# Kernel tuning notes

Measured on AMD Instinct MI355X. Metric: run time of the kernel, lower is better.

Reference implementation:

```python
import jax, jax.numpy as jnp
import numpy as np

NUM_EXPERTS = 3
SCALING = 8.0 / 8.0  # alpha / r


def setup_inputs() -> dict:
    key = jax.random.key(0)
    ks = jax.random.split(key, 8)
    B, H, W, D = 64, 28, 28, 512
    Dh = 4 * D
    E, K, R = 3, 2, 8
    T = B * H * W
    x = jax.random.normal(ks[0], (B, H, W, D), dtype=jnp.float32)
    W1 = jax.random.normal(ks[1], (D, Dh), dtype=jnp.float32) * (1.0 / D ** 0.5)
    b1 = jnp.zeros((Dh,), dtype=jnp.float32)
    W2 = jax.random.normal(ks[2], (Dh, D), dtype=jnp.float32) * (1.0 / Dh ** 0.5)
    b2 = jnp.zeros((D,), dtype=jnp.float32)
    w_down = jax.random.normal(ks[3], (E, D, R), dtype=jnp.float32) * (1.0 / D ** 0.5)
    # original init is zeros; use small randn so output/grads are non-trivial
    w_up = jax.random.normal(ks[4], (E, R, D), dtype=jnp.float32) * 0.02
    gate_logits = jax.random.normal(ks[5], (T, E), dtype=jnp.float32)
    gate_probs = jax.nn.softmax(gate_logits, axis=-1)
    topk_probs, topk_indices = jax.lax.top_k(gate_probs, K)
    topk_indices = topk_indices.astype(jnp.int64)
    return {"x": x, "W1": W1, "b1": b1, "W2": W2, "b2": b2,
            "w_down": w_down, "w_up": w_up, "gate_probs": gate_probs,
            "topk_probs": topk_probs, "topk_indices": topk_indices}


def reference(x, W1, b1, W2, b2, w_down, w_up, gate_probs, topk_probs, topk_indices):
    # frozen base ConvNeXt MLP (channels-last): Linear -> GELU -> Linear
    orig_out = jax.nn.gelu(jnp.dot(x, W1) + b1, approximate=False) @ W2 + b2

    D = x.shape[-1]
    x_flat = x.reshape(-1, D)  # [T, D]

    # dense per-expert LoRA over all tokens (rank-8, cheap), then mask-combine
    down = jnp.einsum('td,edr->etr', x_flat, w_down)          # [E, T, r]
    up = jnp.einsum('etr,erd->etd', jax.nn.gelu(down, approximate=False), w_up) * SCALING  # [E, T, D]

    # weights[e, t] = sum_k topk_probs[t, k] * (topk_indices[t, k] == e)
    E = w_down.shape[0]
    mask = (topk_indices[None, :, :] == jnp.arange(E)[:, None, None])  # [E, T, K]
    weights = jnp.sum(jnp.where(mask, topk_probs[None], 0.0), axis=-1)  # [E, T]

    moe_out = jnp.einsum('et,etd->td', weights, up).reshape(x.shape)
    return orig_out + moe_out
```

## Files before the change

### kernel.cpp

```cpp
#include <hip/hip_runtime.h>

typedef _Float16 f16;
typedef _Float16 f16x8 __attribute__((ext_vector_type(8)));
typedef _Float16 f16x4 __attribute__((ext_vector_type(4)));
typedef float f32x4 __attribute__((ext_vector_type(4)));

#define TD 512
#define TDH 2048

__device__ __forceinline__ float gelu_fast(float x) {
  float u = x * fmaf(x * x, 0.0713548162f, 1.595769122f);
  float e = __expf(-u);
  return x * __builtin_amdgcn_rcpf(1.0f + e);
}

__device__ __forceinline__ void glds16(const f16* g, f16* l) {
  __builtin_amdgcn_global_load_lds(
      (const __attribute__((address_space(1))) void*)g,
      (__attribute__((address_space(3))) void*)l, 16, 0, 0);
}

__global__ __launch_bounds__(256) void k_conv_x(f16* __restrict__ dst,
                                                const float* __restrict__ src,
                                                int n4) {
  int i = blockIdx.x * 256 + threadIdx.x;
  if (i >= n4) return;
  float4 v = ((const float4*)src)[i];
  f16x4 o = {(f16)v.x, (f16)v.y, (f16)v.z, (f16)v.w};
  ((f16x4*)dst)[i] = o;
}

__global__ void k_trans(f16* __restrict__ dst, const float* __restrict__ src,
                        int R, int C) {
  __shared__ float t[32][33];
  const int bx = blockIdx.x, by = blockIdx.y;
  const int tx = threadIdx.x, ty = threadIdx.y;
#pragma unroll
  for (int s = 0; s < 32; s += 8)
    t[ty + s][tx] = src[(size_t)(by * 32 + ty + s) * C + bx * 32 + tx];
  __syncthreads();
#pragma unroll
  for (int s = 0; s < 32; s += 8)
    dst[(size_t)(bx * 32 + ty + s) * R + by * 32 + tx] = (f16)t[tx][ty + s];
}

__global__ __launch_bounds__(256) void k_wdT(f16* __restrict__ dst,
                                             const float* __restrict__ wd) {
  int i = blockIdx.x * 256 + threadIdx.x;
  int n = i >> 9, k = i & 511;
  float v = (n < 24) ? wd[(size_t)((n >> 3) * 512 + k) * 8 + (n & 7)] : 0.0f;
  dst[i] = (f16)v;
}

__global__ __launch_bounds__(256) void k_wuT(f16* __restrict__ dst,
                                             const float* __restrict__ wu) {
  int i = blockIdx.x * 256 + threadIdx.x;
  int d = i >> 5, er = i & 31;
  float v = (er < 24) ? wu[(size_t)(er >> 3) * 4096 + (er & 7) * 512 + d] : 0.0f;
  dst[i] = (f16)v;
}

template <int EPI>
__global__ __launch_bounds__(256) void k_gemm(
    const f16* __restrict__ A, const f16* __restrict__ B, int Kt, int lda,
    int ldb, const float* __restrict__ bias, f16* __restrict__ Hout, int ldh,
    float* __restrict__ Out, int ldc, const float* __restrict__ tkp,
    const int* __restrict__ tki, const f16* __restrict__ Ag,
    const f16* __restrict__ Bg) {
  __shared__ __align__(16) f16 As[2][128 * 32];
  __shared__ __align__(16) f16 Bs[2][128 * 32];
  const int tid = threadIdx.x;
  const int lane = tid & 63;
  const int w = tid >> 6;
  const int wm = w >> 1, wn = w & 1;
  const int bm = blockIdx.x, bn = blockIdx.y;

  const int c0 = 2 * w;
  const int lrow = lane >> 2;
  const int srow = c0 * 16 + lrow;
  const int skk = ((lane & 3) ^ ((lrow >> 1) & 3)) * 8;
  const f16* gA = A + (size_t)(bm * 128 + srow) * lda + skk;
  const f16* gB = B + (size_t)(bn * 128 + srow) * ldb + skk;
  f16* lA0 = &As[0][c0 * 512];
  f16* lA1 = &As[1][c0 * 512];
  f16* lB0 = &Bs[0][c0 * 512];
  f16* lB1 = &Bs[1][c0 * 512];

  f32x4 acc[4][4] = {};

  const int frow = lane & 15;
  const int swk = (((lane >> 4) ^ ((frow >> 1) & 3))) * 8;

  const int nt = Kt / 32;

  glds16(gA, lA0);
  glds16(gA + (size_t)16 * lda, lA0 + 512);
  glds16(gB, lB0);
  glds16(gB + (size_t)16 * ldb, lB0 + 512);
  __syncthreads();

  for (int t = 0; t < nt; ++t) {
    f16* dA = (t & 1) ? lA0 : lA1;
    f16* dB = (t & 1) ? lB0 : lB1;
    if (t + 1 < nt) {
      const int k = (t + 1) * 32;
      glds16(gA + k, dA);
      glds16(gA + k + (size_t)16 * lda, dA + 512);
      glds16(gB + k, dB);
      glds16(gB + k + (size_t)16 * ldb, dB + 512);
    } else if (EPI == 1) {
      const f16* gAg = Ag + (size_t)(bm * 128 + srow) * 32 + skk;
      const f16* gBg = Bg + (size_t)(bn * 128 + srow) * 32 + skk;
      glds16(gAg, dA);
      glds16(gAg + 512, dA + 512);
      glds16(gBg, dB);
      glds16(gBg + 512, dB + 512);
    }
    const f16* rA = As[t & 1];
    const f16* rB = Bs[t & 1];
    f16x8 af[4], bf[4];
#pragma unroll
    for (int i = 0; i < 4; i++)
      af[i] = *(const f16x8*)&rA[(wm * 64 + i * 16 + frow) * 32 + swk];
#pragma unroll
    for (int j = 0; j < 4; j++)
      bf[j] = *(const f16x8*)&rB[(wn * 64 + j * 16 + frow) * 32 + swk];
#pragma unroll
    for (int i = 0; i < 4; i++)
#pragma unroll
      for (int j = 0; j < 4; j++)
        acc[i][j] = __builtin_amdgcn_mfma_f32_16x16x32_f16(bf[j], af[i],
                                                           acc[i][j], 0, 0, 0);
    __syncthreads();
  }

  if constexpr (EPI == 1) {
    const f16* rA = As[nt & 1];
    const f16* rB = Bs[nt & 1];
    f16x8 af[4], bf[4];
#pragma unroll
    for (int i = 0; i < 4; i++)
      af[i] = *(const f16x8*)&rA[(wm * 64 + i * 16 + frow) * 32 + swk];
#pragma unroll
    for (int j = 0; j < 4; j++)
      bf[j] = *(const f16x8*)&rB[(wn * 64 + j * 16 + frow) * 32 + swk];
#pragma unroll
    for (int i = 0; i < 4; i++)
#pragma unroll
      for (int j = 0; j < 4; j++)
        acc[i][j] = __builtin_amdgcn_mfma_f32_16x16x32_f16(bf[j], af[i],
                                                           acc[i][j], 0, 0, 0);
  }

  const int m0 = wm * 64 + (lane & 15);
  const int n0 = wn * 64 + ((lane >> 4) << 2);

  if constexpr (EPI == 0) {
#pragma unroll
    for (int i = 0; i < 4; i++) {
      const size_t rb = (size_t)(bm * 128 + m0 + i * 16) * ldh + bn * 128 + n0;
#pragma unroll
      for (int j = 0; j < 4; j++) {
        const float4 bb = *(const float4*)&bias[bn * 128 + n0 + j * 16];
        f16x4 o = {(f16)gelu_fast(acc[i][j][0] + bb.x),
                   (f16)gelu_fast(acc[i][j][1] + bb.y),
                   (f16)gelu_fast(acc[i][j][2] + bb.z),
                   (f16)gelu_fast(acc[i][j][3] + bb.w)};
        *(f16x4*)&Hout[rb + j * 16] = o;
      }
    }
  } else if constexpr (EPI == 1) {
#pragma unroll
    for (int i = 0; i < 4; i++) {
      const size_t rb = (size_t)(bm * 128 + m0 + i * 16) * ldc + bn * 128 + n0;
#pragma unroll
      for (int j = 0; j < 4; j++) {
        const float4 bb = *(const float4*)&bias[bn * 128 + n0 + j * 16];
        float4 v = {acc[i][j][0] + bb.x, acc[i][j][1] + bb.y,
                    acc[i][j][2] + bb.z, acc[i][j][3] + bb.w};
        *(float4*)&Out[rb + j * 16] = v;
      }
    }
  } else {
    if (wn == 0) {
#pragma unroll
      for (int i = 0; i < 4; i++) {
        const int m = bm * 128 + m0 + i * 16;
        const int i0 = tki[m * 2], i1 = tki[m * 2 + 1];
        const float p0 = tkp[m * 2], p1 = tkp[m * 2 + 1];
#pragma unroll
        for (int j = 0; j < 2; j++) {
          const int nb = n0 + j * 16;
          const int e = nb >> 3;
          const float wgt = (i0 == e ? p0 : 0.0f) + (i1 == e ? p1 : 0.0f);
          f16x4 o = {(f16)(wgt * gelu_fast(acc[i][j][0])),
                     (f16)(wgt * gelu_fast(acc[i][j][1])),
                     (f16)(wgt * gelu_fast(acc[i][j][2])),
                     (f16)(wgt * gelu_fast(acc[i][j][3]))};
          *(f16x4*)&Hout[(size_t)m * 32 + nb] = o;
        }
      }
    }
  }
}

extern "C" void kernel_launch(void* const* d_in, const int* in_sizes, int n_in,
                              void* d_out, int out_size, void* d_ws,
                              size_t ws_size, hipStream_t stream) {
  const float* x = (const float*)d_in[0];
  const float* W1 = (const float*)d_in[1];
  const float* b1 = (const float*)d_in[2];
  const float* W2 = (const float*)d_in[3];
  const float* b2 = (const float*)d_in[4];
  const float* wd = (const float*)d_in[5];
  const float* wu = (const float*)d_in[6];
  const float* tkp = (const float*)d_in[8];
  const int* tki = (const int*)d_in[9];
  float* out = (float*)d_out;

  const int T = in_sizes[0] / TD;

  char* p = (char*)d_ws;
  f16* W1T = (f16*)p; p += (size_t)TDH * TD * sizeof(f16);
  f16* W2T = (f16*)p; p += (size_t)TD * TDH * sizeof(f16);
  f16* wdT = (f16*)p; p += (size_t)128 * TD * sizeof(f16);
  f16* wuT = (f16*)p; p += (size_t)TD * 32 * sizeof(f16);
  size_t fixed = (size_t)(p - (char*)d_ws);
  const size_t per_tok = (size_t)(TD + TDH + 32) * sizeof(f16);
  long mc = (long)((ws_size > fixed ? ws_size - fixed : 0) / per_tok);
  if (mc > T) mc = T;
  mc = (mc / 128) * 128;
  if (mc < 128) mc = 128;
  f16* xb = (f16*)p; p += (size_t)mc * TD * sizeof(f16);
  f16* Hb = (f16*)p; p += (size_t)mc * TDH * sizeof(f16);
  f16* gb = (f16*)p;

  k_trans<<<dim3(TDH / 32, TD / 32), dim3(32, 8), 0, stream>>>(W1T, W1, TD, TDH);
  k_trans<<<dim3(TD / 32, TDH / 32), dim3(32, 8), 0, stream>>>(W2T, W2, TDH, TD);
  k_wdT<<<dim3(65536 / 256), 256, 0, stream>>>(wdT, wd);
  k_wuT<<<dim3(16384 / 256), 256, 0, stream>>>(wuT, wu);

  for (long off = 0; off < T; off += mc) {
    long m = T - off;
    if (m > mc) m = mc;
    const int mt = (int)(m / 128);
    const int n4 = (int)(m * TD / 4);
    k_conv_x<<<dim3((n4 + 255) / 256), 256, 0, stream>>>(xb, x + off * TD, n4);
    k_gemm<2><<<dim3(mt, 1), 256, 0, stream>>>(xb, wdT, TD, TD, TD, nullptr,
                                               gb, 32, nullptr, 0,
                                               tkp + off * 2, tki + off * 2,
                                               nullptr, nullptr);
    k_gemm<0><<<dim3(mt, TDH / 128), 256, 0, stream>>>(
        xb, W1T, TD, TD, TD, b1, Hb, TDH, nullptr, 0, nullptr, nullptr,
        nullptr, nullptr);
    k_gemm<1><<<dim3(mt, TD / 128), 256, 0, stream>>>(
        Hb, W2T, TDH, TDH, TDH, b2, nullptr, 0, out + off * TD, TD, nullptr,
        nullptr, gb, wuT);
  }
}
```

Baseline: 564.8 us.

## Use 256x256 tiled 512-thread GEMM with triple-buffered LDS for the MLP GEMMs

Adds a new GEMM kernel with 256x256 output tiles, 8 waves per block and a three-stage global_load_lds pipeline synchronised by explicit vmcnt waits and barriers. It replaces the 128x128 double-buffered kernel for the W1 (GELU) and W2 (+LoRA up) GEMMs, and swaps the grid order so N tiles vary fastest. The aim is more data reuse per LDS load and better latency hiding. The cost is higher register pressure (128 accumulator floats per thread), 96 KB of LDS, and fewer blocks per chunk. The old kernel is kept only for the rank-32 LoRA down projection.

```diff
diff --git a/kernel.cpp b/kernel.cpp
--- a/kernel.cpp
+++ b/kernel.cpp
@@ -19,6 +19,11 @@
       (const __attribute__((address_space(1))) void*)g,
       (__attribute__((address_space(3))) void*)l, 16, 0, 0);
 }
+
+#define WAITB(N) \
+  asm volatile("s_waitcnt vmcnt(" #N ")\n\ts_barrier" ::: "memory")
+#define DRAINB() \
+  asm volatile("s_waitcnt lgkmcnt(0)\n\ts_barrier" ::: "memory")
 
 __global__ __launch_bounds__(256) void k_conv_x(f16* __restrict__ dst,
                                                 const float* __restrict__ src,
@@ -61,12 +66,129 @@
 }
 
 template <int EPI>
+__global__ __launch_bounds__(512) void k_gemm256(
+    const f16* __restrict__ A, const f16* __restrict__ B, int nt, int lda,
+    int ldb, const float* __restrict__ bias, f16* __restrict__ Hout, int ldh,
+    float* __restrict__ Out, int ldc, const f16* __restrict__ Ag,
+    const f16* __restrict__ Bg) {
+  __shared__ __align__(16) f16 As[3][8192];
+  __shared__ __align__(16) f16 Bs[3][8192];
+  const int tid = threadIdx.x;
+  const int lane = tid & 63;
+  const int w = tid >> 6;
+  const int wm = w >> 2;
+  const int wn = w & 3;
+  const int bn = blockIdx.x, bm = blockIdx.y;
+
+  const int lrow = tid >> 2;
+  const int scol = ((tid & 3) ^ ((lrow >> 1) & 3)) * 8;
+  const f16* pA0 = A + (size_t)(bm * 256 + lrow) * lda + scol;
+  const f16* pA1 = pA0 + (size_t)128 * lda;
+  const f16* pB0 = B + (size_t)(bn * 256 + lrow) * ldb + scol;
+  const f16* pB1 = pB0 + (size_t)128 * ldb;
+  const f16* qA0 = nullptr; const f16* qA1 = nullptr;
+  const f16* qB0 = nullptr; const f16* qB1 = nullptr;
+  if constexpr (EPI == 1) {
+    qA0 = Ag + (size_t)(bm * 256 + lrow) * 32 + scol;
+    qA1 = qA0 + 128 * 32;
+    qB0 = Bg + (size_t)(bn * 256 + lrow) * 32 + scol;
+    qB1 = qB0 + 128 * 32;
+  }
+  const int dbase = w * 512;
+
+  const int ntt = nt + (EPI == 1 ? 1 : 0);
+
+#define STAGE(S, BUF)                                                   \
+  do {                                                                  \
+    f16* dA = &As[BUF][dbase];                                          \
+    f16* dB = &Bs[BUF][dbase];                                          \
+    if ((S) < nt) {                                                     \
+      const size_t o = (size_t)(S) * 32;                                \
+      glds16(pA0 + o, dA); glds16(pA1 + o, dA + 4096);                  \
+      glds16(pB0 + o, dB); glds16(pB1 + o, dB + 4096);                  \
+    } else {                                                            \
+      glds16(qA0, dA); glds16(qA1, dA + 4096);                          \
+      glds16(qB0, dB); glds16(qB1, dB + 4096);                          \
+    }                                                                   \
+  } while (0)
+
+  f32x4 acc[8][4] = {};
+  const int frow = lane & 15;
+  const int swk = (((lane >> 4) ^ ((frow >> 1) & 3))) * 8;
+
+#define COMPUTE(BUF)                                                        \
+  do {                                                                      \
+    const f16* rA = &As[BUF][(wm * 128 + frow) * 32 + swk];                 \
+    const f16* rB = &Bs[BUF][(wn * 64 + frow) * 32 + swk];                  \
+    f16x8 af[8], bf[4];                                                     \
+    _Pragma("unroll") for (int i = 0; i < 8; i++)                           \
+        af[i] = *(const f16x8*)&rA[i * 512];                                \
+    _Pragma("unroll") for (int j = 0; j < 4; j++)                           \
+        bf[j] = *(const f16x8*)&rB[j * 512];                                \
+    _Pragma("unroll") for (int i = 0; i < 8; i++)                           \
+        _Pragma("unroll") for (int j = 0; j < 4; j++)                       \
+            acc[i][j] = __builtin_amdgcn_mfma_f32_16x16x32_f16(             \
+                bf[j], af[i], acc[i][j], 0, 0, 0);                          \
+  } while (0)
+
+  STAGE(0, 0);
+  STAGE(1, 1);
+  STAGE(2, 2);
+
+  int buf = 0;
+  for (int t = 0; t < ntt - 2; ++t) {
+    WAITB(8);
+    COMPUTE(buf);
+    DRAINB();
+    if (t + 3 < ntt) STAGE(t + 3, buf);
+    buf = (buf == 2) ? 0 : buf + 1;
+  }
+  WAITB(4);
+  COMPUTE(buf);
+  DRAINB();
+  buf = (buf == 2) ? 0 : buf + 1;
+  WAITB(0);
+  COMPUTE(buf);
+
+  const int m0 = wm * 128 + (lane & 15);
+  const int n0 = wn * 64 + ((lane >> 4) << 2);
+
+  if constexpr (EPI == 0) {
+#pragma unroll
+    for (int i = 0; i < 8; i++) {
+      const size_t rb = (size_t)(bm * 256 + m0 + i * 16) * ldh + bn * 256 + n0;
+#pragma unroll
+      for (int j = 0; j < 4; j++) {
+        const float4 bb = *(const float4*)&bias[bn * 256 + n0 + j * 16];
+        f16x4 o = {(f16)gelu_fast(acc[i][j][0] + bb.x),
+                   (f16)gelu_fast(acc[i][j][1] + bb.y),
+                   (f16)gelu_fast(acc[i][j][2] + bb.z),
+                   (f16)gelu_fast(acc[i][j][3] + bb.w)};
+        *(f16x4*)&Hout[rb + j * 16] = o;
+      }
+    }
+  } else {
+#pragma unroll
+    for (int i = 0; i < 8; i++) {
+      const size_t rb = (size_t)(bm * 256 + m0 + i * 16) * ldc + bn * 256 + n0;
+#pragma unroll
+      for (int j = 0; j < 4; j++) {
+        const float4 bb = *(const float4*)&bias[bn * 256 + n0 + j * 16];
+        float4 v = {acc[i][j][0] + bb.x, acc[i][j][1] + bb.y,
+                    acc[i][j][2] + bb.z, acc[i][j][3] + bb.w};
+        *(float4*)&Out[rb + j * 16] = v;
+      }
+    }
+  }
+#undef STAGE
+#undef COMPUTE
+}
+
+template <int EPI>
 __global__ __launch_bounds__(256) void k_gemm(
     const f16* __restrict__ A, const f16* __restrict__ B, int Kt, int lda,
-    int ldb, const float* __restrict__ bias, f16* __restrict__ Hout, int ldh,
-    float* __restrict__ Out, int ldc, const float* __restrict__ tkp,
-    const int* __restrict__ tki, const f16* __restrict__ Ag,
-    const f16* __restrict__ Bg) {
+    int ldb, f16* __restrict__ Hout, const float* __restrict__ tkp,
+    const int* __restrict__ tki) {
   __shared__ __align__(16) f16 As[2][128 * 32];
   __shared__ __align__(16) f16 Bs[2][128 * 32];
   const int tid = threadIdx.x;
@@ -87,10 +209,8 @@
   f16* lB1 = &Bs[1][c0 * 512];
 
   f32x4 acc[4][4] = {};
-
   const int frow = lane & 15;
   const int swk = (((lane >> 4) ^ ((frow >> 1) & 3))) * 8;
-
   const int nt = Kt / 32;
 
   glds16(gA, lA0);
@@ -108,13 +228,6 @@
       glds16(gA + k + (size_t)16 * lda, dA + 512);
       glds16(gB + k, dB);
       glds16(gB + k + (size_t)16 * ldb, dB + 512);
-    } else if (EPI == 1) {
-      const f16* gAg = Ag + (size_t)(bm * 128 + srow) * 32 + skk;
-      const f16* gBg = Bg + (size_t)(bn * 128 + srow) * 32 + skk;
-      glds16(gAg, dA);
-      glds16(gAg + 512, dA + 512);
-      glds16(gBg, dB);
-      glds16(gBg + 512, dB + 512);
     }
     const f16* rA = As[t & 1];
     const f16* rB = Bs[t & 1];
@@ -134,71 +247,24 @@
     __syncthreads();
   }
 
-  if constexpr (EPI == 1) {
-    const f16* rA = As[nt & 1];
-    const f16* rB = Bs[nt & 1];
-    f16x8 af[4], bf[4];
-#pragma unroll
-    for (int i = 0; i < 4; i++)
-      af[i] = *(const f16x8*)&rA[(wm * 64 + i * 16 + frow) * 32 + swk];
-#pragma unroll
-    for (int j = 0; j < 4; j++)
-      bf[j] = *(const f16x8*)&rB[(wn * 64 + j * 16 + frow) * 32 + swk];
-#pragma unroll
-    for (int i = 0; i < 4; i++)
-#pragma unroll
-      for (int j = 0; j < 4; j++)
-        acc[i][j] = __builtin_amdgcn_mfma_f32_16x16x32_f16(bf[j], af[i],
-                                                           acc[i][j], 0, 0, 0);
-  }
-
   const int m0 = wm * 64 + (lane & 15);
   const int n0 = wn * 64 + ((lane >> 4) << 2);
-
-  if constexpr (EPI == 0) {
+  if (wn == 0) {
 #pragma unroll
     for (int i = 0; i < 4; i++) {
-      const size_t rb = (size_t)(bm * 128 + m0 + i * 16) * ldh + bn * 128 + n0;
-#pragma unroll
-      for (int j = 0; j < 4; j++) {
-        const float4 bb = *(const float4*)&bias[bn * 128 + n0 + j * 16];
-        f16x4 o = {(f16)gelu_fast(acc[i][j][0] + bb.x),
-                   (f16)gelu_fast(acc[i][j][1] + bb.y),
-                   (f16)gelu_fast(acc[i][j][2] + bb.z),
-                   (f16)gelu_fast(acc[i][j][3] + bb.w)};
-        *(f16x4*)&Hout[rb + j * 16] = o;
-      }
-    }
-  } else if constexpr (EPI == 1) {
-#pragma unroll
-    for (int i = 0; i < 4; i++) {
-      const size_t rb = (size_t)(bm * 128 + m0 + i * 16) * ldc + bn * 128 + n0;
-#pragma unroll
-      for (int j = 0; j < 4; j++) {
-        const float4 bb = *(const float4*)&bias[bn * 128 + n0 + j * 16];
-        float4 v = {acc[i][j][0] + bb.x, acc[i][j][1] + bb.y,
-                    acc[i][j][2] + bb.z, acc[i][j][3] + bb.w};
-        *(float4*)&Out[rb + j * 16] = v;
-      }
-    }
-  } else {
-    if (wn == 0) {
-#pragma unroll
-      for (int i = 0; i < 4; i++) {
-        const int m = bm * 128 + m0 + i * 16;
-        const int i0 = tki[m * 2], i1 = tki[m * 2 + 1];
-        const float p0 = tkp[m * 2], p1 = tkp[m * 2 + 1];
-#pragma unroll
-        for (int j = 0; j < 2; j++) {
-          const int nb = n0 + j * 16;
-          const int e = nb >> 3;
-          const float wgt = (i0 == e ? p0 : 0.0f) + (i1 == e ? p1 : 0.0f);
-          f16x4 o = {(f16)(wgt * gelu_fast(acc[i][j][0])),
-                     (f16)(wgt * gelu_fast(acc[i][j][1])),
-                     (f16)(wgt * gelu_fast(acc[i][j][2])),
-                     (f16)(wgt * gelu_fast(acc[i][j][3]))};
-          *(f16x4*)&Hout[(size_t)m * 32 + nb] = o;
-        }
+      const int m = bm * 128 + m0 + i * 16;
+      const int i0 = tki[m * 2], i1 = tki[m * 2 + 1];
+      const float p0 = tkp[m * 2], p1 = tkp[m * 2 + 1];
+#pragma unroll
+      for (int j = 0; j < 2; j++) {
+        const int nb = n0 + j * 16;
+        const int e = nb >> 3;
+        const float wgt = (i0 == e ? p0 : 0.0f) + (i1 == e ? p1 : 0.0f);
+        f16x4 o = {(f16)(wgt * gelu_fast(acc[i][j][0])),
+                   (f16)(wgt * gelu_fast(acc[i][j][1])),
+                   (f16)(wgt * gelu_fast(acc[i][j][2])),
+                   (f16)(wgt * gelu_fast(acc[i][j][3]))};
+        *(f16x4*)&Hout[(size_t)m * 32 + nb] = o;
       }
     }
   }
@@ -229,8 +295,8 @@
   const size_t per_tok = (size_t)(TD + TDH + 32) * sizeof(f16);
   long mc = (long)((ws_size > fixed ? ws_size - fixed : 0) / per_tok);
   if (mc > T) mc = T;
-  mc = (mc / 128) * 128;
-  if (mc < 128) mc = 128;
+  mc = (mc / 256) * 256;
+  if (mc < 256) mc = 256;
   f16* xb = (f16*)p; p += (size_t)mc * TD * sizeof(f16);
   f16* Hb = (f16*)p; p += (size_t)mc * TDH * sizeof(f16);
   f16* gb = (f16*)p;
@@ -243,18 +309,16 @@
   for (long off = 0; off < T; off += mc) {
     long m = T - off;
     if (m > mc) m = mc;
-    const int mt = (int)(m / 128);
+    const int mt1 = (int)(m / 128);
+    const int mt2 = (int)(m / 256);
     const int n4 = (int)(m * TD / 4);
     k_conv_x<<<dim3((n4 + 255) / 256), 256, 0, stream>>>(xb, x + off * TD, n4);
-    k_gemm<2><<<dim3(mt, 1), 256, 0, stream>>>(xb, wdT, TD, TD, TD, nullptr,
-                                               gb, 32, nullptr, 0,
-                                               tkp + off * 2, tki + off * 2,
-                                               nullptr, nullptr);
-    k_gemm<0><<<dim3(mt, TDH / 128), 256, 0, stream>>>(
-        xb, W1T, TD, TD, TD, b1, Hb, TDH, nullptr, 0, nullptr, nullptr,
-        nullptr, nullptr);
-    k_gemm<1><<<dim3(mt, TD / 128), 256, 0, stream>>>(
-        Hb, W2T, TDH, TDH, TDH, b2, nullptr, 0, out + off * TD, TD, nullptr,
-        nullptr, gb, wuT);
-  }
-}
+    k_gemm<2><<<dim3(mt1, 1), 256, 0, stream>>>(xb, wdT, TD, TD, TD, gb,
+                                                tkp + off * 2, tki + off * 2);
+    k_gemm256<0><<<dim3(TDH / 256, mt2), 512, 0, stream>>>(
+        xb, W1T, TD / 32, TD, TD, b1, Hb, TDH, nullptr, 0, nullptr, nullptr);
+    k_gemm256<1><<<dim3(TD / 256, mt2), 512, 0, stream>>>(
+        Hb, W2T, TDH / 32, TDH, TDH, b2, nullptr, 0, out + off * TD, TD, gb,
+        wuT);
+  }
+}
```

After: 622.3 us. 10.2% more time.

## Replace main GEMMs with 256x256 8-wave ping-pong pipelined kernel and XCD swizzle

Applied to the files above, without the earlier changes.

Replaces the 128x128 double-buffered GEMM used for the two large MLP matmuls with a 512-thread, 256x256-tile kernel. It splits each 64-wide K step into half-tiles, interleaves LDS reads, async global-to-LDS loads and MFMA quarter-blocks behind explicit vmcnt waits and barriers, and raises wave priority around the MFMA bursts. Block indices are remapped so neighbouring tiles land on the same XCD. The LoRA up-projection tail is padded to K=64 so it fits the new K step, which means the lora-down kernel now writes zero padding. The changes target latency hiding and reuse per byte loaded, at the cost of hand-tuned wait counts that are fragile, and the token chunk size must now be a multiple of 256.

```diff
diff --git a/kernel.cpp b/kernel.cpp
--- a/kernel.cpp
+++ b/kernel.cpp
@@ -19,6 +19,19 @@
       (const __attribute__((address_space(1))) void*)g,
       (__attribute__((address_space(3))) void*)l, 16, 0, 0);
 }
+
+#define VW6_BAR()                                          \
+  do {                                                     \
+    asm volatile("s_waitcnt vmcnt(6)" ::: "memory");       \
+    __builtin_amdgcn_s_barrier();                          \
+  } while (0)
+#define VW0_BAR()                                          \
+  do {                                                     \
+    asm volatile("s_waitcnt vmcnt(0)" ::: "memory");       \
+    __builtin_amdgcn_s_barrier();                          \
+  } while (0)
+#define BAR() __builtin_amdgcn_s_barrier()
+#define LGKM0() asm volatile("s_waitcnt lgkmcnt(0)" ::: "memory")
 
 __global__ __launch_bounds__(256) void k_conv_x(f16* __restrict__ dst,
                                                 const float* __restrict__ src,
@@ -55,42 +68,198 @@
 __global__ __launch_bounds__(256) void k_wuT(f16* __restrict__ dst,
                                              const float* __restrict__ wu) {
   int i = blockIdx.x * 256 + threadIdx.x;
-  int d = i >> 5, er = i & 31;
+  int d = i >> 6, er = i & 63;
   float v = (er < 24) ? wu[(size_t)(er >> 3) * 4096 + (er & 7) * 512 + d] : 0.0f;
   dst[i] = (f16)v;
 }
 
 template <int EPI>
-__global__ __launch_bounds__(256) void k_gemm(
+__global__ __launch_bounds__(512, 2) void k_gemm8p(
+    const f16* __restrict__ A, const f16* __restrict__ B, int ntm, int NT,
+    int lda, int ldb, const float* __restrict__ bias, f16* __restrict__ Hout,
+    int ldh, float* __restrict__ Out, int ldc, const f16* __restrict__ Ag,
+    const f16* __restrict__ Bg, int nbn) {
+  __shared__ __align__(16) f16 LA[2][2][8192];
+  __shared__ __align__(16) f16 LB[2][2][8192];
+  const int tid = threadIdx.x;
+  const int lane = tid & 63;
+  const int w = tid >> 6;
+  const int wm = w >> 2, wn = w & 3;
+
+  const int nwg = gridDim.x;
+  const int q = nwg >> 3, r = nwg & 7;
+  const int xcd = blockIdx.x & 7, pos = blockIdx.x >> 3;
+  const int swz =
+      (xcd < r ? xcd * (q + 1) : r * (q + 1) + (xcd - r) * q) + pos;
+  const int bm = swz / nbn, bn = swz - bm * nbn;
+
+  const int lrow = tid >> 2;
+  const int scol = ((tid & 3) ^ ((lrow >> 1) & 3)) * 8;
+  const f16* pA = A + (size_t)(bm * 256 + lrow) * lda + scol;
+  const f16* pB = B + (size_t)(bn * 256 + lrow) * ldb + scol;
+  const f16* qA =
+      (EPI == 1) ? Ag + (size_t)(bm * 256 + lrow) * 64 + scol : nullptr;
+  const f16* qB =
+      (EPI == 1) ? Bg + (size_t)(bn * 256 + lrow) * 64 + scol : nullptr;
+  const int dbase = w * 512;
+  const size_t ldas = (size_t)128 * lda, ldbs = (size_t)128 * ldb;
+
+#define STG_A(S, H, BUF)                                             \
+  do {                                                               \
+    if ((S) < NT) {                                                  \
+      f16* d0 = &LA[BUF][H][dbase];                                  \
+      if ((S) < ntm) {                                               \
+        const f16* s_ = pA + (size_t)(S)*64 + (H)*32;                \
+        glds16(s_, d0);                                              \
+        glds16(s_ + ldas, d0 + 4096);                                \
+      } else {                                                       \
+        const f16* s_ = qA + (H)*32;                                 \
+        glds16(s_, d0);                                              \
+        glds16(s_ + 128 * 64, d0 + 4096);                            \
+      }                                                              \
+    }                                                                \
+  } while (0)
+#define STG_B(S, H, BUF)                                             \
+  do {                                                               \
+    if ((S) < NT) {                                                  \
+      f16* d0 = &LB[BUF][H][dbase];                                  \
+      if ((S) < ntm) {                                               \
+        const f16* s_ = pB + (size_t)(S)*64 + (H)*32;                \
+        glds16(s_, d0);                                              \
+        glds16(s_ + ldbs, d0 + 4096);                                \
+      } else {                                                       \
+        const f16* s_ = qB + (H)*32;                                 \
+        glds16(s_, d0);                                              \
+        glds16(s_ + 128 * 64, d0 + 4096);                            \
+      }                                                              \
+    }                                                                \
+  } while (0)
+
+  f32x4 acc[8][4] = {};
+  f16x8 af[8], bf[4];
+  const int frow = lane & 15;
+  const int swk = ((lane >> 4) ^ ((frow >> 1) & 3)) * 8;
+  const int aoff = (wm * 128 + frow) * 32 + swk;
+  const int boff = (wn * 64 + frow) * 32 + swk;
+
+#define DS_AF(BUF, H)                                           \
+  _Pragma("unroll") for (int i = 0; i < 8; i++) af[i] =         \
+      *(const f16x8*)&LA[BUF][H][aoff + i * 512];
+#define DS_BF(BUF, H, J0)                                       \
+  bf[J0] = *(const f16x8*)&LB[BUF][H][boff + (J0)*512];         \
+  bf[(J0) + 1] = *(const f16x8*)&LB[BUF][H][boff + ((J0) + 1) * 512];
+#define MFQ(NQ)                                                         \
+  __builtin_amdgcn_s_setprio(1);                                        \
+  _Pragma("unroll") for (int i = 0; i < 8; i++) {                       \
+    acc[i][2 * (NQ)] = __builtin_amdgcn_mfma_f32_16x16x32_f16(          \
+        bf[2 * (NQ)], af[i], acc[i][2 * (NQ)], 0, 0, 0);                \
+    acc[i][2 * (NQ) + 1] = __builtin_amdgcn_mfma_f32_16x16x32_f16(      \
+        bf[2 * (NQ) + 1], af[i], acc[i][2 * (NQ) + 1], 0, 0, 0);        \
+  }                                                                     \
+  __builtin_amdgcn_s_setprio(0);
+
+#define ITER(I, W4, W8)                                                    \
+  do {                                                                     \
+    const int t0 = 2 * (I), t1 = t0 + 1;                                   \
+     DS_AF(0, 0); DS_BF(0, 0, 0); STG_B(t1, 1, 1);                  \
+    BAR(); LGKM0(); MFQ(0); BAR();                                         \
+     DS_BF(0, 0, 2); STG_A(t0 + 2, 0, 0);                           \
+    BAR(); LGKM0(); MFQ(1); BAR();                                         \
+     DS_AF(0, 1); DS_BF(0, 1, 0); STG_B(t0 + 2, 0, 0);              \
+    BAR(); LGKM0(); MFQ(0); BAR();                                         \
+     DS_BF(0, 1, 2); STG_A(t0 + 2, 1, 0);                           \
+    W4(); LGKM0(); MFQ(1); BAR();                                          \
+     DS_AF(1, 0); DS_BF(1, 0, 0); STG_B(t0 + 2, 1, 0);              \
+    BAR(); LGKM0(); MFQ(0); BAR();                                         \
+     DS_BF(1, 0, 2); STG_A(t1 + 2, 0, 1);                           \
+    BAR(); LGKM0(); MFQ(1); BAR();                                         \
+     DS_AF(1, 1); DS_BF(1, 1, 0); STG_B(t1 + 2, 0, 1);              \
+    BAR(); LGKM0(); MFQ(0); BAR();                                         \
+     DS_BF(1, 1, 2); STG_A(t1 + 2, 1, 1);                           \
+    W8(); LGKM0(); MFQ(1); BAR();                                          \
+  } while (0)
+
+  STG_A(0, 0, 0); STG_B(0, 0, 0); STG_A(0, 1, 0); STG_B(0, 1, 0);
+  STG_A(1, 0, 1); STG_B(1, 0, 1); STG_A(1, 1, 1);
+  VW6_BAR();
+
+  const int NIT = NT >> 1;
+#pragma unroll 1
+  for (int i = 0; i + 1 < NIT; ++i) ITER(i, VW6_BAR, VW6_BAR);
+  if constexpr (EPI == 0) {
+    ITER(NIT - 1, VW0_BAR, VW0_BAR);
+  } else {
+    ITER(NIT - 1, VW6_BAR, VW0_BAR);
+    DS_AF(0, 0); DS_BF(0, 0, 0); LGKM0(); MFQ(0);
+    DS_BF(0, 0, 2); LGKM0(); MFQ(1);
+    DS_AF(0, 1); DS_BF(0, 1, 0); LGKM0(); MFQ(0);
+    DS_BF(0, 1, 2); LGKM0(); MFQ(1);
+  }
+
+  const int m0 = wm * 128 + (lane & 15);
+  const int n0 = wn * 64 + ((lane >> 4) << 2);
+
+  if constexpr (EPI == 0) {
+#pragma unroll
+    for (int i = 0; i < 8; i++) {
+      const size_t rb = (size_t)(bm * 256 + m0 + i * 16) * ldh + bn * 256 + n0;
+#pragma unroll
+      for (int j = 0; j < 4; j++) {
+        const float4 bb = *(const float4*)&bias[bn * 256 + n0 + j * 16];
+        f16x4 o = {(f16)gelu_fast(acc[i][j][0] + bb.x),
+                   (f16)gelu_fast(acc[i][j][1] + bb.y),
+                   (f16)gelu_fast(acc[i][j][2] + bb.z),
+                   (f16)gelu_fast(acc[i][j][3] + bb.w)};
+        *(f16x4*)&Hout[rb + j * 16] = o;
+      }
+    }
+  } else {
+#pragma unroll
+    for (int i = 0; i < 8; i++) {
+      const size_t rb = (size_t)(bm * 256 + m0 + i * 16) * ldc + bn * 256 + n0;
+#pragma unroll
+      for (int j = 0; j < 4; j++) {
+        const float4 bb = *(const float4*)&bias[bn * 256 + n0 + j * 16];
+        float4 v = {acc[i][j][0] + bb.x, acc[i][j][1] + bb.y,
+                    acc[i][j][2] + bb.z, acc[i][j][3] + bb.w};
+        *(float4*)&Out[rb + j * 16] = v;
+      }
+    }
+  }
+#undef STG_A
+#undef STG_B
+#undef DS_AF
+#undef DS_BF
+#undef MFQ
+#undef ITER
+}
+
+__global__ __launch_bounds__(256) void k_lora_down(
     const f16* __restrict__ A, const f16* __restrict__ B, int Kt, int lda,
-    int ldb, const float* __restrict__ bias, f16* __restrict__ Hout, int ldh,
-    float* __restrict__ Out, int ldc, const float* __restrict__ tkp,
-    const int* __restrict__ tki, const f16* __restrict__ Ag,
-    const f16* __restrict__ Bg) {
+    int ldb, f16* __restrict__ Gout, const float* __restrict__ tkp,
+    const int* __restrict__ tki) {
   __shared__ __align__(16) f16 As[2][128 * 32];
   __shared__ __align__(16) f16 Bs[2][128 * 32];
   const int tid = threadIdx.x;
   const int lane = tid & 63;
   const int w = tid >> 6;
   const int wm = w >> 1, wn = w & 1;
-  const int bm = blockIdx.x, bn = blockIdx.y;
+  const int bm = blockIdx.x;
 
   const int c0 = 2 * w;
   const int lrow = lane >> 2;
   const int srow = c0 * 16 + lrow;
   const int skk = ((lane & 3) ^ ((lrow >> 1) & 3)) * 8;
   const f16* gA = A + (size_t)(bm * 128 + srow) * lda + skk;
-  const f16* gB = B + (size_t)(bn * 128 + srow) * ldb + skk;
+  const f16* gB = B + (size_t)srow * ldb + skk;
   f16* lA0 = &As[0][c0 * 512];
   f16* lA1 = &As[1][c0 * 512];
   f16* lB0 = &Bs[0][c0 * 512];
   f16* lB1 = &Bs[1][c0 * 512];
 
   f32x4 acc[4][4] = {};
-
   const int frow = lane & 15;
-  const int swk = (((lane >> 4) ^ ((frow >> 1) & 3))) * 8;
-
+  const int swk = ((lane >> 4) ^ ((frow >> 1) & 3)) * 8;
   const int nt = Kt / 32;
 
   glds16(gA, lA0);
@@ -108,13 +277,6 @@
       glds16(gA + k + (size_t)16 * lda, dA + 512);
       glds16(gB + k, dB);
       glds16(gB + k + (size_t)16 * ldb, dB + 512);
-    } else if (EPI == 1) {
-      const f16* gAg = Ag + (size_t)(bm * 128 + srow) * 32 + skk;
-      const f16* gBg = Bg + (size_t)(bn * 128 + srow) * 32 + skk;
-      glds16(gAg, dA);
-      glds16(gAg + 512, dA + 512);
-      glds16(gBg, dB);
-      glds16(gBg + 512, dB + 512);
     }
     const f16* rA = As[t & 1];
     const f16* rB = Bs[t & 1];
@@ -134,71 +296,26 @@
     __syncthreads();
   }
 
-  if constexpr (EPI == 1) {
-    const f16* rA = As[nt & 1];
-    const f16* rB = Bs[nt & 1];
-    f16x8 af[4], bf[4];
-#pragma unroll
-    for (int i = 0; i < 4; i++)
-      af[i] = *(const f16x8*)&rA[(wm * 64 + i * 16 + frow) * 32 + swk];
-#pragma unroll
-    for (int j = 0; j < 4; j++)
-      bf[j] = *(const f16x8*)&rB[(wn * 64 + j * 16 + frow) * 32 + swk];
-#pragma unroll
-    for (int i = 0; i < 4; i++)
-#pragma unroll
-      for (int j = 0; j < 4; j++)
-        acc[i][j] = __builtin_amdgcn_mfma_f32_16x16x32_f16(bf[j], af[i],
-                                                           acc[i][j], 0, 0, 0);
-  }
-
   const int m0 = wm * 64 + (lane & 15);
   const int n0 = wn * 64 + ((lane >> 4) << 2);
-
-  if constexpr (EPI == 0) {
+  if (wn == 0) {
 #pragma unroll
     for (int i = 0; i < 4; i++) {
-      const size_t rb = (size_t)(bm * 128 + m0 + i * 16) * ldh + bn * 128 + n0;
-#pragma unroll
-      for (int j = 0; j < 4; j++) {
-        const float4 bb = *(const float4*)&bias[bn * 128 + n0 + j * 16];
-        f16x4 o = {(f16)gelu_fast(acc[i][j][0] + bb.x),
-                   (f16)gelu_fast(acc[i][j][1] + bb.y),
-                   (f16)gelu_fast(acc[i][j][2] + bb.z),
-                   (f16)gelu_fast(acc[i][j][3] + bb.w)};
-        *(f16x4*)&Hout[rb + j * 16] = o;
-      }
-    }
-  } else if constexpr (EPI == 1) {
-#pragma unroll
-    for (int i = 0; i < 4; i++) {
-      const size_t rb = (size_t)(bm * 128 + m0 + i * 16) * ldc + bn * 128 + n0;
-#pragma unroll
-      for (int j = 0; j < 4; j++) {
-        const float4 bb = *(const float4*)&bias[bn * 128 + n0 + j * 16];
-        float4 v = {acc[i][j][0] + bb.x, acc[i][j][1] + bb.y,
-                    acc[i][j][2] + bb.z, acc[i][j][3] + bb.w};
-        *(float4*)&Out[rb + j * 16] = v;
-      }
-    }
-  } else {
-    if (wn == 0) {
-#pragma unroll
-      for (int i = 0; i < 4; i++) {
-        const int m = bm * 128 + m0 + i * 16;
-        const int i0 = tki[m * 2], i1 = tki[m * 2 + 1];
-        const float p0 = tkp[m * 2], p1 = tkp[m * 2 + 1];
-#pragma unroll
-        for (int j = 0; j < 2; j++) {
-          const int nb = n0 + j * 16;
-          const int e = nb >> 3;
-          const float wgt = (i0 == e ? p0 : 0.0f) + (i1 == e ? p1 : 0.0f);
-          f16x4 o = {(f16)(wgt * gelu_fast(acc[i][j][0])),
-                     (f16)(wgt * gelu_fast(acc[i][j][1])),
-                     (f16)(wgt * gelu_fast(acc[i][j][2])),
-                     (f16)(wgt * gelu_fast(acc[i][j][3]))};
-          *(f16x4*)&Hout[(size_t)m * 32 + nb] = o;
-        }
+      const int m = bm * 128 + m0 + i * 16;
+      const int i0 = tki[m * 2], i1 = tki[m * 2 + 1];
+      const float p0 = tkp[m * 2], p1 = tkp[m * 2 + 1];
+#pragma unroll
+      for (int j = 0; j < 2; j++) {
+        const int nb = n0 + j * 16;
+        const int e = nb >> 3;
+        const float wgt = (i0 == e ? p0 : 0.0f) + (i1 == e ? p1 : 0.0f);
+        f16x4 o = {(f16)(wgt * gelu_fast(acc[i][j][0])),
+                   (f16)(wgt * gelu_fast(acc[i][j][1])),
+                   (f16)(wgt * gelu_fast(acc[i][j][2])),
+                   (f16)(wgt * gelu_fast(acc[i][j][3]))};
+        *(f16x4*)&Gout[(size_t)m * 64 + nb] = o;
+        f16x4 z = {(f16)0.f, (f16)0.f, (f16)0.f, (f16)0.f};
+        *(f16x4*)&Gout[(size_t)m * 64 + nb + 32] = z;
       }
     }
   }
@@ -224,37 +341,38 @@
   f16* W1T = (f16*)p; p += (size_t)TDH * TD * sizeof(f16);
   f16* W2T = (f16*)p; p += (size_t)TD * TDH * sizeof(f16);
   f16* wdT = (f16*)p; p += (size_t)128 * TD * sizeof(f16);
-  f16* wuT = (f16*)p; p += (size_t)TD * 32 * sizeof(f16);
+  f16* wuT = (f16*)p; p += (size_t)TD * 64 * sizeof(f16);
   size_t fixed = (size_t)(p - (char*)d_ws);
-  const size_t per_tok = (size_t)(TD + TDH + 32) * sizeof(f16);
+  const size_t per_tok = (size_t)(TD + TDH + 64) * sizeof(f16);
   long mc = (long)((ws_size > fixed ? ws_size - fixed : 0) / per_tok);
   if (mc > T) mc = T;
-  mc = (mc / 128) * 128;
-  if (mc < 128) mc = 128;
+  mc = (mc / 256) * 256;
+  if (mc < 256) mc = 256;
   f16* xb = (f16*)p; p += (size_t)mc * TD * sizeof(f16);
   f16* Hb = (f16*)p; p += (size_t)mc * TDH * sizeof(f16);
   f16* gb = (f16*)p;
 
-  k_trans<<<dim3(TDH / 32, TD / 32), dim3(32, 8), 0, stream>>>(W1T, W1, TD, TDH);
-  k_trans<<<dim3(TD / 32, TDH / 32), dim3(32, 8), 0, stream>>>(W2T, W2, TDH, TD);
+  k_trans<<<dim3(TDH / 32, TD / 32), dim3(32, 8), 0, stream>>>(W1T, W1, TD,
+                                                               TDH);
+  k_trans<<<dim3(TD / 32, TDH / 32), dim3(32, 8), 0, stream>>>(W2T, W2, TDH,
+                                                               TD);
   k_wdT<<<dim3(65536 / 256), 256, 0, stream>>>(wdT, wd);
-  k_wuT<<<dim3(16384 / 256), 256, 0, stream>>>(wuT, wu);
+  k_wuT<<<dim3(32768 / 256), 256, 0, stream>>>(wuT, wu);
 
   for (long off = 0; off < T; off += mc) {
     long m = T - off;
     if (m > mc) m = mc;
-    const int mt = (int)(m / 128);
+    const int mt1 = (int)(m / 128);
+    const int mt2 = (int)(m / 256);
     const int n4 = (int)(m * TD / 4);
     k_conv_x<<<dim3((n4 + 255) / 256), 256, 0, stream>>>(xb, x + off * TD, n4);
-    k_gemm<2><<<dim3(mt, 1), 256, 0, stream>>>(xb, wdT, TD, TD, TD, nullptr,
-                                               gb, 32, nullptr, 0,
-                                               tkp + off * 2, tki + off * 2,
-                                               nullptr, nullptr);
-    k_gemm<0><<<dim3(mt, TDH / 128), 256, 0, stream>>>(
-        xb, W1T, TD, TD, TD, b1, Hb, TDH, nullptr, 0, nullptr, nullptr,
-        nullptr, nullptr);
-    k_gemm<1><<<dim3(mt, TD / 128), 256, 0, stream>>>(
-        Hb, W2T, TDH, TDH, TDH, b2, nullptr, 0, out + off * TD, TD, nullptr,
-        nullptr, gb, wuT);
-  }
-}
+    k_lora_down<<<dim3(mt1), 256, 0, stream>>>(xb, wdT, TD, TD, TD, gb,
+                                               tkp + off * 2, tki + off * 2);
+    k_gemm8p<0><<<dim3(mt2 * (TDH / 256)), 512, 0, stream>>>(
+        xb, W1T, TD / 64, TD / 64, TD, TD, b1, Hb, TDH, nullptr, 0, nullptr,
+        nullptr, TDH / 256);
+    k_gemm8p<1><<<dim3(mt2 * (TD / 256)), 512, 0, stream>>>(
+        Hb, W2T, TDH / 64, TDH / 64 + 1, TDH, TDH, b2, nullptr, 0,
+        out + off * TD, TD, gb, wuT, TD / 256);
+  }
+}
```

Measured after the change: 550.0 us. 2.6% less time.
